# Performance work log

Hardware: AMD Instinct MI355X
Metric: run time of the kernel (lower is better)

## Reference

```python
import jax, jax.numpy as jnp
import numpy as np

B, S, H, NH = 2, 2048, 1024, 16
HD = H // NH
SCALE = float(H) ** 0.5  # note: source scales by sqrt(hidden_dim), not sqrt(head_dim)
EPS = 1e-5


def setup_inputs() -> dict:
    key = jax.random.key(0)
    ks = jax.random.split(key, 16)
    s = 0.02
    return {
        "q": jax.random.normal(ks[0], (B, S, H), jnp.float32),
        "k": jax.random.normal(ks[1], (B, S, H), jnp.float32),
        "v": jax.random.normal(ks[2], (B, S, H), jnp.float32),
        "mask": jax.random.randint(ks[3], (B, 1, S, S), 0, 2, jnp.int32),
        "Wq": jax.random.normal(ks[4], (H, H), jnp.float32) * s,
        "bq": jnp.zeros((H,), jnp.float32),
        "Wk": jax.random.normal(ks[5], (H, H), jnp.float32) * s,
        "bk": jnp.zeros((H,), jnp.float32),
        "Wv": jax.random.normal(ks[6], (H, H), jnp.float32) * s,
        "bv": jnp.zeros((H,), jnp.float32),
        "Wfc": jax.random.normal(ks[7], (H, H), jnp.float32) * s,
        "bfc": jnp.zeros((H,), jnp.float32),
        "gamma": jnp.ones((H,), jnp.float32),
        "beta": jnp.zeros((H,), jnp.float32),
    }


def reference(q, k, v, mask, Wq, bq, Wk, bk, Wv, bv, Wfc, bfc, gamma, beta):
    residual = q
    qh = (q @ Wq + bq).reshape(B, S, NH, HD)
    kh = (k @ Wk + bk).reshape(B, S, NH, HD)
    vh = (v @ Wv + bv).reshape(B, S, NH, HD)
    # full [B, NH, S, S] score matrix, as in the source
    energy = jnp.einsum('nqhd,nkhd->nhqk', qh, kh)
    energy = jnp.where(mask == 0, jnp.float32(-1e9), energy)
    attn = jax.nn.softmax(energy / SCALE, axis=3)  # dropout p=0.0 -> identity
    out = jnp.einsum('nhqk,nkhd->nqhd', attn, vh).reshape(B, S, H)
    y = out @ Wfc + bfc + residual
    mu = jnp.mean(y, axis=-1, keepdims=True)
    var = jnp.mean((y - mu) ** 2, axis=-1, keepdims=True)
    return gamma * (y - mu) / jnp.sqrt(var + EPS) + beta
```

## Files before the change

kernel.cpp:

```cpp
#include <hip/hip_runtime.h>
#include <hip/hip_bf16.h>

#define S_LEN  2048
#define HDIM   1024
#define NHEADS 16
#define HEADD  64
#define BATCH  2
#define MTOT   (BATCH * S_LEN)
#define K2EXP  0.04508422f

typedef __attribute__((ext_vector_type(8)))  __bf16 bf16x8;
typedef __attribute__((ext_vector_type(4)))  __bf16 bf16x4;
typedef __attribute__((ext_vector_type(4)))  float  f32x4;
typedef __attribute__((ext_vector_type(16))) float  f32x16;

__device__ __forceinline__ void gload16(const void* g, void* l) {
  __builtin_amdgcn_global_load_lds(
      (const __attribute__((address_space(1))) void*)g,
      (__attribute__((address_space(3))) void*)l, 16, 0, 0);
}
__device__ __forceinline__ bf16x8 lds_rd(const __bf16* base, int row, int bcol) {
  const char* p = (const char*)base + row * 128 + (bcol ^ ((row & 7) << 4));
  return *(const bf16x8*)p;
}
__device__ __forceinline__ unsigned cvtpk_bf16(float lo, float hi) {
  unsigned r;
  asm("v_cvt_pk_bf16_f32 %0, %1, %2" : "=v"(r) : "v"(lo), "v"(hi));
  return r;
}
__device__ __forceinline__ void plswap(unsigned& a, unsigned& b) {
  asm volatile("v_permlane32_swap_b32 %0, %1" : "+v"(a), "+v"(b));
}

__global__ __launch_bounds__(256)
void cvt_kernel(const float* __restrict__ q, const float* __restrict__ k,
                const float* __restrict__ v, __bf16* __restrict__ Qc,
                __bf16* __restrict__ Kc, __bf16* __restrict__ Vc)
{
  const int z = blockIdx.z;
  const float* src = (z == 0) ? q : (z == 1) ? k : v;
  __bf16* dst = (z == 0) ? Qc : (z == 1) ? Kc : Vc;
  const size_t i = ((size_t)blockIdx.x * 256 + threadIdx.x) * 8;
  const float4 a = *(const float4*)&src[i];
  const float4 c = *(const float4*)&src[i + 4];
  bf16x8 o;
  o[0] = (__bf16)a.x; o[1] = (__bf16)a.y; o[2] = (__bf16)a.z; o[3] = (__bf16)a.w;
  o[4] = (__bf16)c.x; o[5] = (__bf16)c.y; o[6] = (__bf16)c.z; o[7] = (__bf16)c.w;
  *(bf16x8*)&dst[i] = o;
}

__global__ __launch_bounds__(256)
void maskpack_kernel(const int* __restrict__ mask, unsigned* __restrict__ mbT)
{
  const size_t idx = (size_t)blockIdx.x * 256 + threadIdx.x;
  const int m = mask[idx];
  const unsigned long long bal = __ballot(m != 0);
  if ((threadIdx.x & 63) == 0) {
    const int b   = (int)(idx >> 22);
    const int qq  = (int)(idx >> 11) & 2047;
    const int kvw = ((int)idx & 2047) >> 5;
    mbT[((size_t)b * 64 + kvw) * S_LEN + qq]       = (unsigned)bal;
    mbT[((size_t)b * 64 + kvw + 1) * S_LEN + qq]   = (unsigned)(bal >> 32);
  }
}

__global__ __launch_bounds__(256)
void transw_kernel(const float* __restrict__ Wq, const float* __restrict__ Wk,
                   const float* __restrict__ Wv, const float* __restrict__ Wfc,
                   __bf16* __restrict__ Wt)
{
  __shared__ float T[64][65];
  const int z = blockIdx.z;
  const float* W = (z == 0) ? Wq : (z == 1) ? Wk : (z == 2) ? Wv : Wfc;
  const float sc = (z == 0) ? K2EXP : 1.0f;
  __bf16* O = Wt + (size_t)z * HDIM * HDIM;
  const int k0 = blockIdx.x * 64, n0 = blockIdx.y * 64;
  const int tid = threadIdx.x;
  const int r  = tid >> 4;
  const int c4 = (tid & 15) * 4;
  #pragma unroll
  for (int p = 0; p < 4; ++p) {
    const int row = r + p * 16;
    const float4 vv = *(const float4*)&W[(size_t)(k0 + row) * HDIM + n0 + c4];
    T[row][c4 + 0] = vv.x; T[row][c4 + 1] = vv.y;
    T[row][c4 + 2] = vv.z; T[row][c4 + 3] = vv.w;
  }
  __syncthreads();
  #pragma unroll
  for (int p = 0; p < 4; ++p) {
    const int n = r + p * 16;
    bf16x4 o;
    #pragma unroll
    for (int i = 0; i < 4; ++i) o[i] = (__bf16)(T[c4 + i][n] * sc);
    *(bf16x4*)&O[(size_t)(n0 + n) * HDIM + k0 + c4] = o;
  }
}

template<int MODE>
__device__ __forceinline__ void gemm_body(
    const __bf16* __restrict__ A, const __bf16* __restrict__ Wt,
    const float* __restrict__ bias, float bscale,
    const float* __restrict__ resid,
    __bf16* __restrict__ Ob, float* __restrict__ Of, __bf16* __restrict__ Vtg)
{
  __shared__ __bf16 As[2][128][64];
  __shared__ __bf16 Bs[2][128][64];
  const int tid = threadIdx.x, lane = tid & 63, w = tid >> 6;
  const int fr = lane & 15, k8 = (lane >> 4) * 8;
  const int wr = w >> 1, wc = w & 1;
  const int f   = blockIdx.x + gridDim.x * blockIdx.y;
  const int cpx = (gridDim.x * gridDim.y) >> 3;
  const int fs  = (f & 7) * cpx + (f >> 3);
  const int m0 = (fs / gridDim.x) * 128, n0 = (fs % gridDim.x) * 128;
  const int srow8 = lane >> 3, slot = lane & 7;

  f32x4 acc[4][4] = {};

  #define G_STAGE(kt, bf)                                                    \
    {                                                                        \
      _Pragma("unroll")                                                      \
      for (int c = 0; c < 4; ++c) {                                          \
        const int ra = w * 32 + c * 8 + srow8;                               \
        gload16(&A[(size_t)(m0 + ra) * HDIM + (kt) * 64 + ((slot ^ (ra & 7)) * 8)], \
                (void*)&As[bf][w * 32 + c * 8][0]);                          \
      }                                                                      \
      _Pragma("unroll")                                                      \
      for (int c = 0; c < 4; ++c) {                                          \
        const int rb = w * 32 + c * 8 + srow8;                               \
        gload16(&Wt[(size_t)(n0 + rb) * HDIM + (kt) * 64 + ((slot ^ (rb & 7)) * 8)], \
                (void*)&Bs[bf][w * 32 + c * 8][0]);                          \
      }                                                                      \
    }

  #define G_COMPUTE(bf)                                                      \
    {                                                                        \
      _Pragma("unroll")                                                      \
      for (int kk = 0; kk < 64; kk += 32) {                                  \
        bf16x8 a[4], b[4];                                                   \
        _Pragma("unroll")                                                    \
        for (int i = 0; i < 4; ++i)                                          \
          a[i] = lds_rd(&As[bf][0][0], wr * 64 + i * 16 + fr, (kk + k8) * 2);\
        _Pragma("unroll")                                                    \
        for (int j = 0; j < 4; ++j)                                          \
          b[j] = lds_rd(&Bs[bf][0][0], wc * 64 + j * 16 + fr, (kk + k8) * 2);\
        _Pragma("unroll")                                                    \
        for (int i = 0; i < 4; ++i)                                          \
          _Pragma("unroll")                                                  \
          for (int j = 0; j < 4; ++j)                                        \
            acc[i][j] = __builtin_amdgcn_mfma_f32_16x16x32_bf16(a[i], b[j], acc[i][j], 0, 0, 0); \
      }                                                                      \
    }

  G_STAGE(0, 0)
  for (int kt = 0; kt < 15; ++kt) {
    G_STAGE(kt + 1, (kt + 1) & 1)
    asm volatile("s_waitcnt vmcnt(8)" ::: "memory");
    __builtin_amdgcn_s_barrier();
    __builtin_amdgcn_sched_barrier(0);
    __builtin_amdgcn_s_setprio(1);
    G_COMPUTE(kt & 1)
    __builtin_amdgcn_s_setprio(0);
    __builtin_amdgcn_sched_barrier(0);
    __builtin_amdgcn_s_barrier();
  }
  asm volatile("s_waitcnt vmcnt(0)" ::: "memory");
  __builtin_amdgcn_s_barrier();
  G_COMPUTE(1)

  const int rg = (lane >> 4) * 4;
  #pragma unroll
  for (int i = 0; i < 4; ++i) {
    #pragma unroll
    for (int j = 0; j < 4; ++j) {
      const int col = n0 + wc * 64 + j * 16 + fr;
      if constexpr (MODE == 2) {
        const int h = col >> 6, hd = col & 63;
        const int row = m0 + wr * 64 + i * 16 + rg;
        const int bq = row >> 11, qq = row & 2047;
        bf16x4 o;
        #pragma unroll
        for (int r = 0; r < 4; ++r) o[r] = (__bf16)(acc[i][j][r] + bias[col]);
        *(bf16x4*)&Vtg[(((size_t)bq * NHEADS + h) * HEADD + hd) * S_LEN + qq] = o;
      } else {
        #pragma unroll
        for (int r = 0; r < 4; ++r) {
          const int row = m0 + wr * 64 + i * 16 + rg + r;
          if constexpr (MODE == 0) {
            Ob[(size_t)row * HDIM + col] = (__bf16)(acc[i][j][r] + bias[col] * bscale);
          } else {
            Of[(size_t)row * HDIM + col] =
                acc[i][j][r] + bias[col] + resid[(size_t)row * HDIM + col];
          }
        }
      }
    }
  }
  #undef G_STAGE
  #undef G_COMPUTE
}

__global__ __launch_bounds__(256)
void qk_kernel(const __bf16* __restrict__ Qc, const __bf16* __restrict__ Kc,
               const __bf16* __restrict__ Wt,
               const float* __restrict__ bq, const float* __restrict__ bk,
               __bf16* __restrict__ Qb, __bf16* __restrict__ Kb)
{
  const int z = blockIdx.z;
  gemm_body<0>(z ? Kc : Qc, Wt + (size_t)z * HDIM * HDIM, z ? bk : bq,
               z ? 1.0f : K2EXP, nullptr, z ? Kb : Qb, nullptr, nullptr);
}

__global__ __launch_bounds__(256)
void vproj_kernel(const __bf16* __restrict__ Vc, const __bf16* __restrict__ Wt,
                  const float* __restrict__ bv, __bf16* __restrict__ Vtg)
{
  gemm_body<2>(Vc, Wt + (size_t)2 * HDIM * HDIM, bv, 1.0f, nullptr,
               nullptr, nullptr, Vtg);
}

__global__ __launch_bounds__(256)
void fc_kernel(const __bf16* __restrict__ A, const __bf16* __restrict__ Wt,
               const float* __restrict__ bias, const float* __restrict__ resid,
               float* __restrict__ Of)
{
  gemm_body<1>(A, Wt + (size_t)3 * HDIM * HDIM, bias, 1.0f, resid,
               nullptr, Of, nullptr);
}

__global__ __launch_bounds__(256)
void attn_kernel(const __bf16* __restrict__ Qb, const __bf16* __restrict__ Kb,
                 const __bf16* __restrict__ Vtg, const unsigned* __restrict__ mbT,
                 __bf16* __restrict__ AO)
{
  __shared__ __bf16 Ks[2][64][64];
  __shared__ __bf16 Vt[2][64][64];
  __shared__ __align__(16) float Lsm[4][32];

  const int bh = blockIdx.x, b = bh >> 4, h = bh & 15;
  const int tid = threadIdx.x, lane = tid & 63, w = tid >> 6;
  const int fr = lane & 31, hi = lane >> 5;
  const int qw = blockIdx.y * 128 + w * 32;
  const int q  = qw + fr;

  bf16x8 qf[4];
  #pragma unroll
  for (int st = 0; st < 4; ++st)
    qf[st] = *(const bf16x8*)&Qb[((size_t)b * S_LEN + q) * HDIM + h * HEADD + st * 16 + hi * 8];

  const int srow = w * 16 + (lane >> 3), slot = lane & 7;
  const __bf16* ksrc = Kb  + ((size_t)b * S_LEN + srow) * HDIM + h * HEADD + (slot ^ (srow & 7)) * 8;
  const __bf16* vsrc = Vtg + ((size_t)bh * HEADD + srow) * S_LEN + (slot ^ (srow & 7)) * 8;
  const unsigned* mrow = mbT + (size_t)b * 64 * S_LEN + q;

  f32x16 o0 = {}, o1 = {};
  float lsum = 0.f;
  unsigned mv0, mv1, nv0 = 0, nv1 = 0;

  mv0 = mrow[0];
  mv1 = mrow[S_LEN];
  gload16(ksrc,            (void*)&Ks[0][w * 16][0]);
  gload16(ksrc + 8 * HDIM, (void*)&Ks[0][w * 16 + 8][0]);
  gload16(vsrc,             (void*)&Vt[0][w * 16][0]);
  gload16(vsrc + 8 * S_LEN, (void*)&Vt[0][w * 16 + 8][0]);

  for (int t = 0; t < 32; ++t) {
    const int buf = t & 1;
    if (t < 31) {
      nv0 = mrow[(size_t)(2 * t + 2) * S_LEN];
      nv1 = mrow[(size_t)(2 * t + 3) * S_LEN];
      const __bf16* kp = ksrc + (size_t)(t + 1) * 64 * HDIM;
      const __bf16* vp = vsrc + (t + 1) * 64;
      gload16(kp,            (void*)&Ks[buf ^ 1][w * 16][0]);
      gload16(kp + 8 * HDIM, (void*)&Ks[buf ^ 1][w * 16 + 8][0]);
      gload16(vp,             (void*)&Vt[buf ^ 1][w * 16][0]);
      gload16(vp + 8 * S_LEN, (void*)&Vt[buf ^ 1][w * 16 + 8][0]);
      asm volatile("s_waitcnt vmcnt(6)" ::: "memory");
    } else {
      asm volatile("s_waitcnt vmcnt(0)" ::: "memory");
    }
    __builtin_amdgcn_s_barrier();
    __builtin_amdgcn_sched_barrier(0);

    f32x16 s0 = {}, s1 = {};
    __builtin_amdgcn_s_setprio(1);
    #pragma unroll
    for (int st = 0; st < 4; ++st) {
      const bf16x8 ka0 = lds_rd(&Ks[buf][0][0], fr,      st * 32 + hi * 16);
      const bf16x8 ka1 = lds_rd(&Ks[buf][0][0], 32 + fr, st * 32 + hi * 16);
      s0 = __builtin_amdgcn_mfma_f32_32x32x16_bf16(ka0, qf[st], s0, 0, 0, 0);
      s1 = __builtin_amdgcn_mfma_f32_32x32x16_bf16(ka1, qf[st], s1, 0, 0, 0);
    }
    __builtin_amdgcn_s_setprio(0);

    float pp[32];
    const int kb = 4 * hi;
    #pragma unroll
    for (int j = 0; j < 16; ++j) {
      const int kvl = (j & 3) + 8 * (j >> 2) + kb;
      const float e0 = __builtin_amdgcn_exp2f(s0[j]);
      const float e1 = __builtin_amdgcn_exp2f(s1[j]);
      pp[j]      = ((mv0 >> kvl) & 1u) ? e0 : 0.f;
      pp[16 + j] = ((mv1 >> kvl) & 1u) ? e1 : 0.f;
      lsum += pp[j] + pp[16 + j];
    }

    bf16x8 pa[4];
    #pragma unroll
    for (int g = 0; g < 4; ++g) {
      const int o = (g >> 1) * 16 + (g & 1) * 8;
      unsigned x  = cvtpk_bf16(pp[o + 0], pp[o + 1]);
      unsigned x2 = cvtpk_bf16(pp[o + 2], pp[o + 3]);
      unsigned y  = cvtpk_bf16(pp[o + 4], pp[o + 5]);
      unsigned y2 = cvtpk_bf16(pp[o + 6], pp[o + 7]);
      plswap(x, y);
      plswap(x2, y2);
      union { unsigned u[4]; bf16x8 v; } uu;
      uu.u[0] = x; uu.u[1] = x2; uu.u[2] = y; uu.u[3] = y2;
      pa[g] = uu.v;
    }

    __builtin_amdgcn_s_setprio(1);
    #pragma unroll
    for (int g = 0; g < 4; ++g) {
      const bf16x8 vb0 = lds_rd(&Vt[buf][0][0], fr,      g * 32 + hi * 16);
      const bf16x8 vb1 = lds_rd(&Vt[buf][0][0], 32 + fr, g * 32 + hi * 16);
      o0 = __builtin_amdgcn_mfma_f32_32x32x16_bf16(pa[g], vb0, o0, 0, 0, 0);
      o1 = __builtin_amdgcn_mfma_f32_32x32x16_bf16(pa[g], vb1, o1, 0, 0, 0);
    }
    __builtin_amdgcn_s_setprio(0);

    mv0 = nv0; mv1 = nv1;
    __builtin_amdgcn_sched_barrier(0);
    __builtin_amdgcn_s_barrier();
  }

  const float lt = lsum + __shfl_xor(lsum, 32);
  if (hi == 0) Lsm[w][fr] = lt;
  #pragma unroll
  for (int g = 0; g < 4; ++g) {
    const f32x4 L = *(const f32x4*)&Lsm[w][g * 8 + hi * 4];
    #pragma unroll
    for (int r = 0; r < 4; ++r) {
      const float inv = __builtin_amdgcn_rcpf(L[r]);
      const int j = g * 4 + r;
      const int qq = qw + g * 8 + hi * 4 + r;
      AO[((size_t)b * S_LEN + qq) * HDIM + h * HEADD + fr]      = (__bf16)(o0[j] * inv);
      AO[((size_t)b * S_LEN + qq) * HDIM + h * HEADD + 32 + fr] = (__bf16)(o1[j] * inv);
    }
  }
}

__global__ __launch_bounds__(256)
void ln_kernel(float* __restrict__ y, const float* __restrict__ gamma,
               const float* __restrict__ beta)
{
  __shared__ float red[8];
  const int tid = threadIdx.x;
  float* p = y + (size_t)blockIdx.x * HDIM;

  float4 vv = *(const float4*)&p[tid * 4];
  float s  = vv.x + vv.y + vv.z + vv.w;
  float ss = vv.x * vv.x + vv.y * vv.y + vv.z * vv.z + vv.w * vv.w;
  #pragma unroll
  for (int d = 1; d < 64; d <<= 1) {
    s  += __shfl_xor(s, d);
    ss += __shfl_xor(ss, d);
  }
  const int wid = tid >> 6;
  if ((tid & 63) == 0) { red[wid * 2] = s; red[wid * 2 + 1] = ss; }
  __syncthreads();
  s  = red[0] + red[2] + red[4] + red[6];
  ss = red[1] + red[3] + red[5] + red[7];
  const float mean = s * (1.0f / HDIM);
  const float var  = ss * (1.0f / HDIM) - mean * mean;
  const float inv  = rsqrtf(var + 1e-5f);

  const float4 g  = *(const float4*)&gamma[tid * 4];
  const float4 bt = *(const float4*)&beta[tid * 4];
  vv.x = (vv.x - mean) * inv * g.x + bt.x;
  vv.y = (vv.y - mean) * inv * g.y + bt.y;
  vv.z = (vv.z - mean) * inv * g.z + bt.z;
  vv.w = (vv.w - mean) * inv * g.w + bt.w;
  *(float4*)&p[tid * 4] = vv;
}

extern "C" void kernel_launch(void* const* d_in, const int* in_sizes, int n_in,
                              void* d_out, int out_size, void* d_ws, size_t ws_size,
                              hipStream_t stream) {
  const float* q     = (const float*)d_in[0];
  const float* k     = (const float*)d_in[1];
  const float* v     = (const float*)d_in[2];
  const int*   mask  = (const int*)  d_in[3];
  const float* Wq    = (const float*)d_in[4];
  const float* bq    = (const float*)d_in[5];
  const float* Wk    = (const float*)d_in[6];
  const float* bk    = (const float*)d_in[7];
  const float* Wv    = (const float*)d_in[8];
  const float* bv    = (const float*)d_in[9];
  const float* Wfc   = (const float*)d_in[10];
  const float* bfc   = (const float*)d_in[11];
  const float* gamma = (const float*)d_in[12];
  const float* beta  = (const float*)d_in[13];
  float* out = (float*)d_out;

  char* ws = (char*)d_ws;
  const size_t MB16 = (size_t)MTOT * HDIM * 2;
  unsigned* mbT = (unsigned*)ws;
  __bf16* Wt  = (__bf16*)(ws + (1u << 20));
  __bf16* Qc  = (__bf16*)(ws + (1u << 20) + 4 * (size_t)HDIM * HDIM * 2);
  __bf16* Kc  = (__bf16*)((char*)Qc + MB16);
  __bf16* Vc  = (__bf16*)((char*)Kc + MB16);
  __bf16* Qb  = (__bf16*)((char*)Vc + MB16);
  __bf16* Kb  = (__bf16*)((char*)Qb + MB16);
  __bf16* Vtg = (__bf16*)((char*)Kb + MB16);
  __bf16* AO  = Kc;

  const dim3 blk(256);

  cvt_kernel<<<dim3(MTOT * HDIM / 8 / 256, 1, 3), blk, 0, stream>>>(q, k, v, Qc, Kc, Vc);
  maskpack_kernel<<<dim3((size_t)BATCH * S_LEN * S_LEN / 256), blk, 0, stream>>>(mask, mbT);
  transw_kernel<<<dim3(16, 16, 4), blk, 0, stream>>>(Wq, Wk, Wv, Wfc, Wt);

  qk_kernel<<<dim3(HDIM / 128, MTOT / 128, 2), blk, 0, stream>>>(
      Qc, Kc, Wt, bq, bk, Qb, Kb);
  vproj_kernel<<<dim3(HDIM / 128, MTOT / 128), blk, 0, stream>>>(
      Vc, Wt, bv, Vtg);

  attn_kernel<<<dim3(BATCH * NHEADS, S_LEN / 128), blk, 0, stream>>>(
      Qb, Kb, Vtg, mbT, AO);

  fc_kernel<<<dim3(HDIM / 128, MTOT / 128), blk, 0, stream>>>(
      AO, Wt, bfc, q, out);

  ln_kernel<<<dim3(MTOT), blk, 0, stream>>>(out, gamma, beta);
}
```

Before: 170.2 us.

## Merge QKV projection launches, shrink FC tile, load attention K/V directly to registers

Three changes land together. The Q/K and V projection kernels become one launch with grid z=3. The FC GEMM uses 64-row M tiles so more blocks cover the GPU. The attention kernel drops its LDS double-buffering and barriers and instead loads K and V fragments straight from global memory into registers, prefetching the next K tile. The goals are fewer launches, better occupancy for the FC GEMM, and no LDS round-trips or barrier stalls in attention, at the cost of more register pressure and uncoalesced or redundant global loads across waves.

Result: slower. 209.0 us (+22.8%).

```diff
diff --git a/kernel.cpp b/kernel.cpp
--- a/kernel.cpp
+++ b/kernel.cpp
@@ -96,39 +96,39 @@
   }
 }
 
-template<int MODE>
+template<int MODE, int BMT>
 __device__ __forceinline__ void gemm_body(
+    __bf16* As, __bf16* Bs,
     const __bf16* __restrict__ A, const __bf16* __restrict__ Wt,
     const float* __restrict__ bias, float bscale,
     const float* __restrict__ resid,
     __bf16* __restrict__ Ob, float* __restrict__ Of, __bf16* __restrict__ Vtg)
 {
-  __shared__ __bf16 As[2][128][64];
-  __shared__ __bf16 Bs[2][128][64];
+  constexpr int AI = BMT / 32;
   const int tid = threadIdx.x, lane = tid & 63, w = tid >> 6;
   const int fr = lane & 15, k8 = (lane >> 4) * 8;
   const int wr = w >> 1, wc = w & 1;
   const int f   = blockIdx.x + gridDim.x * blockIdx.y;
   const int cpx = (gridDim.x * gridDim.y) >> 3;
   const int fs  = (f & 7) * cpx + (f >> 3);
-  const int m0 = (fs / gridDim.x) * 128, n0 = (fs % gridDim.x) * 128;
+  const int m0 = (fs / gridDim.x) * BMT, n0 = (fs % gridDim.x) * 128;
   const int srow8 = lane >> 3, slot = lane & 7;
 
-  f32x4 acc[4][4] = {};
+  f32x4 acc[AI][4] = {};
 
   #define G_STAGE(kt, bf)                                                    \
     {                                                                        \
       _Pragma("unroll")                                                      \
-      for (int c = 0; c < 4; ++c) {                                          \
-        const int ra = w * 32 + c * 8 + srow8;                               \
+      for (int c = 0; c < AI; ++c) {                                         \
+        const int ra = w * (BMT / 4) + c * 8 + srow8;                        \
         gload16(&A[(size_t)(m0 + ra) * HDIM + (kt) * 64 + ((slot ^ (ra & 7)) * 8)], \
-                (void*)&As[bf][w * 32 + c * 8][0]);                          \
+                (void*)&As[((bf) * BMT + ra) * 64]);                         \
       }                                                                      \
       _Pragma("unroll")                                                      \
       for (int c = 0; c < 4; ++c) {                                          \
         const int rb = w * 32 + c * 8 + srow8;                               \
         gload16(&Wt[(size_t)(n0 + rb) * HDIM + (kt) * 64 + ((slot ^ (rb & 7)) * 8)], \
-                (void*)&Bs[bf][w * 32 + c * 8][0]);                          \
+                (void*)&Bs[((bf) * 128 + rb) * 64]);                         \
       }                                                                      \
     }
 
@@ -136,15 +136,15 @@
     {                                                                        \
       _Pragma("unroll")                                                      \
       for (int kk = 0; kk < 64; kk += 32) {                                  \
-        bf16x8 a[4], b[4];                                                   \
+        bf16x8 a[AI], b[4];                                                  \
         _Pragma("unroll")                                                    \
-        for (int i = 0; i < 4; ++i)                                          \
-          a[i] = lds_rd(&As[bf][0][0], wr * 64 + i * 16 + fr, (kk + k8) * 2);\
+        for (int i = 0; i < AI; ++i)                                         \
+          a[i] = lds_rd(&As[(bf) * BMT * 64], wr * (BMT / 2) + i * 16 + fr, (kk + k8) * 2); \
         _Pragma("unroll")                                                    \
         for (int j = 0; j < 4; ++j)                                          \
-          b[j] = lds_rd(&Bs[bf][0][0], wc * 64 + j * 16 + fr, (kk + k8) * 2);\
+          b[j] = lds_rd(&Bs[(bf) * 128 * 64], wc * 64 + j * 16 + fr, (kk + k8) * 2); \
         _Pragma("unroll")                                                    \
-        for (int i = 0; i < 4; ++i)                                          \
+        for (int i = 0; i < AI; ++i)                                         \
           _Pragma("unroll")                                                  \
           for (int j = 0; j < 4; ++j)                                        \
             acc[i][j] = __builtin_amdgcn_mfma_f32_16x16x32_bf16(a[i], b[j], acc[i][j], 0, 0, 0); \
@@ -154,7 +154,8 @@
   G_STAGE(0, 0)
   for (int kt = 0; kt < 15; ++kt) {
     G_STAGE(kt + 1, (kt + 1) & 1)
-    asm volatile("s_waitcnt vmcnt(8)" ::: "memory");
+    if constexpr (BMT == 128) asm volatile("s_waitcnt vmcnt(8)" ::: "memory");
+    else                      asm volatile("s_waitcnt vmcnt(6)" ::: "memory");
     __builtin_amdgcn_s_barrier();
     __builtin_amdgcn_sched_barrier(0);
     __builtin_amdgcn_s_setprio(1);
@@ -169,13 +170,13 @@
 
   const int rg = (lane >> 4) * 4;
   #pragma unroll
-  for (int i = 0; i < 4; ++i) {
+  for (int i = 0; i < AI; ++i) {
     #pragma unroll
     for (int j = 0; j < 4; ++j) {
       const int col = n0 + wc * 64 + j * 16 + fr;
       if constexpr (MODE == 2) {
         const int h = col >> 6, hd = col & 63;
-        const int row = m0 + wr * 64 + i * 16 + rg;
+        const int row = m0 + wr * (BMT / 2) + i * 16 + rg;
         const int bq = row >> 11, qq = row & 2047;
         bf16x4 o;
         #pragma unroll
@@ -184,7 +185,7 @@
       } else {
         #pragma unroll
         for (int r = 0; r < 4; ++r) {
-          const int row = m0 + wr * 64 + i * 16 + rg + r;
+          const int row = m0 + wr * (BMT / 2) + i * 16 + rg + r;
           if constexpr (MODE == 0) {
             Ob[(size_t)row * HDIM + col] = (__bf16)(acc[i][j][r] + bias[col] * bscale);
           } else {
@@ -200,22 +201,25 @@
 }
 
 __global__ __launch_bounds__(256)
-void qk_kernel(const __bf16* __restrict__ Qc, const __bf16* __restrict__ Kc,
-               const __bf16* __restrict__ Wt,
-               const float* __restrict__ bq, const float* __restrict__ bk,
-               __bf16* __restrict__ Qb, __bf16* __restrict__ Kb)
-{
+void qkv_kernel(const __bf16* __restrict__ Qc, const __bf16* __restrict__ Kc,
+                const __bf16* __restrict__ Vc, const __bf16* __restrict__ Wt,
+                const float* __restrict__ bq, const float* __restrict__ bk,
+                const float* __restrict__ bv,
+                __bf16* __restrict__ Qb, __bf16* __restrict__ Kb,
+                __bf16* __restrict__ Vtg)
+{
+  __shared__ __bf16 smem[2 * 128 * 64 * 2];
+  __bf16* As = smem;
+  __bf16* Bs = smem + 2 * 128 * 64;
   const int z = blockIdx.z;
-  gemm_body<0>(z ? Kc : Qc, Wt + (size_t)z * HDIM * HDIM, z ? bk : bq,
-               z ? 1.0f : K2EXP, nullptr, z ? Kb : Qb, nullptr, nullptr);
-}
-
-__global__ __launch_bounds__(256)
-void vproj_kernel(const __bf16* __restrict__ Vc, const __bf16* __restrict__ Wt,
-                  const float* __restrict__ bv, __bf16* __restrict__ Vtg)
-{
-  gemm_body<2>(Vc, Wt + (size_t)2 * HDIM * HDIM, bv, 1.0f, nullptr,
-               nullptr, nullptr, Vtg);
+  if (z == 2) {
+    gemm_body<2, 128>(As, Bs, Vc, Wt + (size_t)2 * HDIM * HDIM, bv, 1.0f,
+                      nullptr, nullptr, nullptr, Vtg);
+  } else {
+    gemm_body<0, 128>(As, Bs, z ? Kc : Qc, Wt + (size_t)z * HDIM * HDIM,
+                      z ? bk : bq, z ? 1.0f : K2EXP, nullptr,
+                      z ? Kb : Qb, nullptr, nullptr);
+  }
 }
 
 __global__ __launch_bounds__(256)
@@ -223,8 +227,11 @@
                const float* __restrict__ bias, const float* __restrict__ resid,
                float* __restrict__ Of)
 {
-  gemm_body<1>(A, Wt + (size_t)3 * HDIM * HDIM, bias, 1.0f, resid,
-               nullptr, Of, nullptr);
+  __shared__ __bf16 smem[2 * 64 * 64 + 2 * 128 * 64];
+  __bf16* As = smem;
+  __bf16* Bs = smem + 2 * 64 * 64;
+  gemm_body<1, 64>(As, Bs, A, Wt + (size_t)3 * HDIM * HDIM, bias, 1.0f, resid,
+                   nullptr, Of, nullptr);
 }
 
 __global__ __launch_bounds__(256)
@@ -232,8 +239,6 @@
                  const __bf16* __restrict__ Vtg, const unsigned* __restrict__ mbT,
                  __bf16* __restrict__ AO)
 {
-  __shared__ __bf16 Ks[2][64][64];
-  __shared__ __bf16 Vt[2][64][64];
   __shared__ __align__(16) float Lsm[4][32];
 
   const int bh = blockIdx.x, b = bh >> 4, h = bh & 15;
@@ -247,48 +252,51 @@
   for (int st = 0; st < 4; ++st)
     qf[st] = *(const bf16x8*)&Qb[((size_t)b * S_LEN + q) * HDIM + h * HEADD + st * 16 + hi * 8];
 
-  const int srow = w * 16 + (lane >> 3), slot = lane & 7;
-  const __bf16* ksrc = Kb  + ((size_t)b * S_LEN + srow) * HDIM + h * HEADD + (slot ^ (srow & 7)) * 8;
-  const __bf16* vsrc = Vtg + ((size_t)bh * HEADD + srow) * S_LEN + (slot ^ (srow & 7)) * 8;
+  const __bf16* kb0 = &Kb[((size_t)b * S_LEN + fr) * HDIM + h * HEADD + hi * 8];
+  const __bf16* kb1 = kb0 + (size_t)32 * HDIM;
+  const __bf16* vb0 = &Vtg[((size_t)bh * HEADD + fr) * S_LEN + hi * 8];
+  const __bf16* vb1 = vb0 + (size_t)32 * S_LEN;
   const unsigned* mrow = mbT + (size_t)b * 64 * S_LEN + q;
 
   f32x16 o0 = {}, o1 = {};
   float lsum = 0.f;
-  unsigned mv0, mv1, nv0 = 0, nv1 = 0;
-
-  mv0 = mrow[0];
-  mv1 = mrow[S_LEN];
-  gload16(ksrc,            (void*)&Ks[0][w * 16][0]);
-  gload16(ksrc + 8 * HDIM, (void*)&Ks[0][w * 16 + 8][0]);
-  gload16(vsrc,             (void*)&Vt[0][w * 16][0]);
-  gload16(vsrc + 8 * S_LEN, (void*)&Vt[0][w * 16 + 8][0]);
-
+
+  bf16x8 kc0[4], kc1[4];
+  unsigned mv0 = mrow[0], mv1 = mrow[S_LEN];
+  #pragma unroll
+  for (int st = 0; st < 4; ++st) {
+    kc0[st] = *(const bf16x8*)(kb0 + st * 16);
+    kc1[st] = *(const bf16x8*)(kb1 + st * 16);
+  }
+
+  #pragma unroll 2
   for (int t = 0; t < 32; ++t) {
-    const int buf = t & 1;
+    bf16x8 vc0[4], vc1[4];
+    #pragma unroll
+    for (int g = 0; g < 4; ++g) {
+      vc0[g] = *(const bf16x8*)(vb0 + (size_t)t * 64 + g * 16);
+      vc1[g] = *(const bf16x8*)(vb1 + (size_t)t * 64 + g * 16);
+    }
+    bf16x8 kn0[4], kn1[4];
+    unsigned nm0 = 0, nm1 = 0;
     if (t < 31) {
-      nv0 = mrow[(size_t)(2 * t + 2) * S_LEN];
-      nv1 = mrow[(size_t)(2 * t + 3) * S_LEN];
-      const __bf16* kp = ksrc + (size_t)(t + 1) * 64 * HDIM;
-      const __bf16* vp = vsrc + (t + 1) * 64;
-      gload16(kp,            (void*)&Ks[buf ^ 1][w * 16][0]);
-      gload16(kp + 8 * HDIM, (void*)&Ks[buf ^ 1][w * 16 + 8][0]);
-      gload16(vp,             (void*)&Vt[buf ^ 1][w * 16][0]);
-      gload16(vp + 8 * S_LEN, (void*)&Vt[buf ^ 1][w * 16 + 8][0]);
-      asm volatile("s_waitcnt vmcnt(6)" ::: "memory");
-    } else {
-      asm volatile("s_waitcnt vmcnt(0)" ::: "memory");
-    }
-    __builtin_amdgcn_s_barrier();
-    __builtin_amdgcn_sched_barrier(0);
+      const __bf16* kp0 = kb0 + (size_t)(t + 1) * 64 * HDIM;
+      const __bf16* kp1 = kb1 + (size_t)(t + 1) * 64 * HDIM;
+      #pragma unroll
+      for (int st = 0; st < 4; ++st) {
+        kn0[st] = *(const bf16x8*)(kp0 + st * 16);
+        kn1[st] = *(const bf16x8*)(kp1 + st * 16);
+      }
+      nm0 = mrow[(size_t)(2 * t + 2) * S_LEN];
+      nm1 = mrow[(size_t)(2 * t + 3) * S_LEN];
+    }
 
     f32x16 s0 = {}, s1 = {};
     __builtin_amdgcn_s_setprio(1);
     #pragma unroll
     for (int st = 0; st < 4; ++st) {
-      const bf16x8 ka0 = lds_rd(&Ks[buf][0][0], fr,      st * 32 + hi * 16);
-      const bf16x8 ka1 = lds_rd(&Ks[buf][0][0], 32 + fr, st * 32 + hi * 16);
-      s0 = __builtin_amdgcn_mfma_f32_32x32x16_bf16(ka0, qf[st], s0, 0, 0, 0);
-      s1 = __builtin_amdgcn_mfma_f32_32x32x16_bf16(ka1, qf[st], s1, 0, 0, 0);
+      s0 = __builtin_amdgcn_mfma_f32_32x32x16_bf16(kc0[st], qf[st], s0, 0, 0, 0);
+      s1 = __builtin_amdgcn_mfma_f32_32x32x16_bf16(kc1[st], qf[st], s1, 0, 0, 0);
     }
     __builtin_amdgcn_s_setprio(0);
 
@@ -322,16 +330,14 @@
     __builtin_amdgcn_s_setprio(1);
     #pragma unroll
     for (int g = 0; g < 4; ++g) {
-      const bf16x8 vb0 = lds_rd(&Vt[buf][0][0], fr,      g * 32 + hi * 16);
-      const bf16x8 vb1 = lds_rd(&Vt[buf][0][0], 32 + fr, g * 32 + hi * 16);
-      o0 = __builtin_amdgcn_mfma_f32_32x32x16_bf16(pa[g], vb0, o0, 0, 0, 0);
-      o1 = __builtin_amdgcn_mfma_f32_32x32x16_bf16(pa[g], vb1, o1, 0, 0, 0);
+      o0 = __builtin_amdgcn_mfma_f32_32x32x16_bf16(pa[g], vc0[g], o0, 0, 0, 0);
+      o1 = __builtin_amdgcn_mfma_f32_32x32x16_bf16(pa[g], vc1[g], o1, 0, 0, 0);
     }
     __builtin_amdgcn_s_setprio(0);
 
-    mv0 = nv0; mv1 = nv1;
-    __builtin_amdgcn_sched_barrier(0);
-    __builtin_amdgcn_s_barrier();
+    mv0 = nm0; mv1 = nm1;
+    #pragma unroll
+    for (int st = 0; st < 4; ++st) { kc0[st] = kn0[st]; kc1[st] = kn1[st]; }
   }
 
   const float lt = lsum + __shfl_xor(lsum, 32);
@@ -421,15 +427,13 @@
   maskpack_kernel<<<dim3((size_t)BATCH * S_LEN * S_LEN / 256), blk, 0, stream>>>(mask, mbT);
   transw_kernel<<<dim3(16, 16, 4), blk, 0, stream>>>(Wq, Wk, Wv, Wfc, Wt);
 
-  qk_kernel<<<dim3(HDIM / 128, MTOT / 128, 2), blk, 0, stream>>>(
-      Qc, Kc, Wt, bq, bk, Qb, Kb);
-  vproj_kernel<<<dim3(HDIM / 128, MTOT / 128), blk, 0, stream>>>(
-      Vc, Wt, bv, Vtg);
+  qkv_kernel<<<dim3(HDIM / 128, MTOT / 128, 3), blk, 0, stream>>>(
+      Qc, Kc, Vc, Wt, bq, bk, bv, Qb, Kb, Vtg);
 
   attn_kernel<<<dim3(BATCH * NHEADS, S_LEN / 128), blk, 0, stream>>>(
       Qb, Kb, Vtg, mbT, AO);
 
-  fc_kernel<<<dim3(HDIM / 128, MTOT / 128), blk, 0, stream>>>(
+  fc_kernel<<<dim3(HDIM / 128, MTOT / 64), blk, 0, stream>>>(
       AO, Wt, bfc, q, out);
 
   ln_kernel<<<dim3(MTOT), blk, 0, stream>>>(out, gamma, beta);
```
